# Kernel optimization log

Measured on AMD Instinct MI355X. Metric: run time of the kernel, lower is better.

The kernel has to match this reference:

```python
import jax, jax.numpy as jnp
import numpy as np

T, B, I, H = 2048, 32, 256, 256
KEEP = 0.75  # 1 - dropout_rate


def setup_inputs() -> dict:
    key = jax.random.key(0)
    ks = jax.random.split(key, 7)
    inp = jax.random.normal(ks[0], (T, B, I), dtype=jnp.float32)
    # variational dropout masks sampled once (Bernoulli(keep)), like the torch module
    zx = (jax.random.uniform(ks[1], (I,)) < KEEP).astype(jnp.float32)
    zh = (jax.random.uniform(ks[2], (H,)) < KEEP).astype(jnp.float32)
    # stacked gate weights in order [i, f, o, g]; scaled like nn.Linear default init
    s_w = 1.0 / np.sqrt(I)
    s_u = 1.0 / np.sqrt(H)
    W = jax.random.uniform(ks[3], (4 * H, I), minval=-s_w, maxval=s_w, dtype=jnp.float32)
    bW = jax.random.uniform(ks[4], (4 * H,), minval=-s_w, maxval=s_w, dtype=jnp.float32)
    U = jax.random.uniform(ks[5], (4 * H, H), minval=-s_u, maxval=s_u, dtype=jnp.float32)
    bU = jax.random.uniform(ks[6], (4 * H,), minval=-s_u, maxval=s_u, dtype=jnp.float32)
    return {"input": inp, "zx": zx, "zh": zh, "W": W, "bW": bW, "U": U, "bU": bU}


def reference(input, zx, zh, W, bW, U, bU):
    Bsz = input.shape[1]
    Hd = U.shape[1]

    def step(carry, x_t):
        h, c = carry
        x = x_t * zx          # [B, I] variational input dropout
        hm = h * zh           # [B, H] variational hidden dropout
        gates = x @ W.T + bW + hm @ U.T + bU   # [B, 4H]
        i, f, o, g = jnp.split(gates, 4, axis=-1)
        i = jax.nn.sigmoid(i)
        f = jax.nn.sigmoid(f)
        o = jax.nn.sigmoid(o)
        g = jnp.tanh(g)
        c_new = f * c + i * g
        h_new = o * jnp.tanh(c_new)
        return (h_new, c_new), h_new

    h0 = jnp.zeros((Bsz, Hd), dtype=input.dtype)
    c0 = jnp.zeros((Bsz, Hd), dtype=input.dtype)
    (h_t, c_t), hn = jax.lax.scan(step, (h0, c0), input)
    return hn, h_t, c_t
```

## Files before the change

kernel.cpp:

```cpp
#include <hip/hip_runtime.h>
#include <stdint.h>

typedef _Float16 half_t;
typedef _Float16 half2_t __attribute__((ext_vector_type(2)));
typedef _Float16 half8_t __attribute__((ext_vector_type(8)));
typedef float f32x4 __attribute__((ext_vector_type(4)));

#define TSEQ 2048
#define NB   32
#define HD   256
#define KC   224
#define KH   112
#define NQ   7
#define HN_ELEMS ((size_t)TSEQ*NB*HD)

static __device__ __forceinline__ int sdot4(uint32_t a, uint32_t b, int c) {
#if defined(__has_builtin)
#if __has_builtin(__builtin_amdgcn_sdot4)
  return __builtin_amdgcn_sdot4((int)a, (int)b, c, false);
#else
  int d;
  asm("v_dot4_i32_i8 %0, %1, %2, %3" : "=v"(d) : "v"(a), "v"(b), "v"(c));
  return d;
#endif
#else
  int d;
  asm("v_dot4_i32_i8 %0, %1, %2, %3" : "=v"(d) : "v"(a), "v"(b), "v"(c));
  return d;
#endif
}
static __device__ __forceinline__ float sigm_f(float x) {
  return __builtin_amdgcn_rcpf(1.0f + __expf(-x));
}
static __device__ __forceinline__ float tanh_f(float x) {
  return 2.0f * __builtin_amdgcn_rcpf(1.0f + __expf(-2.0f * x)) - 1.0f;
}
static __device__ __forceinline__ signed char q8(float v, float sc) {
  int q = (int)rintf(v * sc);
  q = q > 127 ? 127 : (q < -127 ? -127 : q);
  return (signed char)q;
}

__global__ void prep_kernel(const float* __restrict__ W, const float* __restrict__ U,
                            const float* __restrict__ bW, const float* __restrict__ bU,
                            const float* __restrict__ zx, const float* __restrict__ zh,
                            half_t* __restrict__ Wf16, signed char* __restrict__ Upk3b,
                            signed char* __restrict__ Ug4b, float* __restrict__ bias,
                            int* __restrict__ ipos,
                            half_t* __restrict__ hstate, float* __restrict__ cstate) {
  int tid = blockIdx.x * 256 + threadIdx.x;
  int n   = tid & 1023;
  int kcG = tid >> 10;

  int p = 0;
  for (int kk = 0; kk < kcG * 8; ++kk) p += (zh[kk] != 0.0f) ? 1 : 0;

  #pragma unroll
  for (int e = 0; e < 8; ++e) {
    int k = kcG * 8 + e;
    Wf16[(size_t)n * 256 + k] = (half_t)(W[n * 256 + k] * zx[k]);
    bool kept = (zh[k] != 0.0f);
    if (n == 0) ipos[k] = (kept && p < KC) ? p : -1;
    if (kept && p < KC) {
      float uv = U[n * 256 + k] * zh[k];
      signed char qv = q8(uv, 2032.0f);
      int kg = p / KH, pp = p % KH, q = pp >> 4, by = pp & 15;
      if (n < 768) {
        int c = n >> 8, j = n & 255;
        Upk3b[(((size_t)(c * 2 + kg) * NQ + q) * 256 + j) * 16 + by] = qv;
      } else {
        Ug4b[(((size_t)kg * NQ + q) * 256 + (n & 255)) * 16 + by] = qv;
      }
    }
    if (kept) ++p;
  }
  if (kcG == 0) bias[n] = bW[n] + bU[n];
  if (tid < NB * HD) { hstate[tid] = (half_t)0.0f; cstate[tid] = 0.0f; }
}

__global__ __launch_bounds__(256)
void gemm_kernel(const float* __restrict__ input, const half_t* __restrict__ Wf16,
                 const float* __restrict__ bias, half_t* __restrict__ gx, int row0) {
  const int tid  = threadIdx.x;
  const int lane = tid & 63;
  const int w    = tid >> 6;
  const int mr   = lane & 15;
  const int g    = lane >> 4;
  const int nb   = (blockIdx.x & 3) * 256;
  const int m0   = (blockIdx.x >> 2) * 64 + w * 16;

  f32x4 acc[16];
  #pragma unroll
  for (int nf = 0; nf < 16; ++nf) acc[nf] = (f32x4){0.f, 0.f, 0.f, 0.f};

  const float* arow = input + ((size_t)(row0 + m0 + mr)) * 256 + g * 8;
  #pragma unroll 1
  for (int kk = 0; kk < 8; ++kk) {
    float4 v0 = ((const float4*)(arow + kk * 32))[0];
    float4 v1 = ((const float4*)(arow + kk * 32))[1];
    half8_t a;
    a[0] = (half_t)v0.x; a[1] = (half_t)v0.y; a[2] = (half_t)v0.z; a[3] = (half_t)v0.w;
    a[4] = (half_t)v1.x; a[5] = (half_t)v1.y; a[6] = (half_t)v1.z; a[7] = (half_t)v1.w;
    const half_t* bbase = Wf16 + (size_t)(nb + mr) * 256 + kk * 32 + g * 8;
    #pragma unroll
    for (int nf = 0; nf < 16; ++nf) {
      uint4 bu = *(const uint4*)(bbase + (size_t)nf * 16 * 256);
      half8_t b = __builtin_bit_cast(half8_t, bu);
      acc[nf] = __builtin_amdgcn_mfma_f32_16x16x32_f16(a, b, acc[nf], 0, 0, 0);
    }
  }

  #pragma unroll
  for (int nf = 0; nf < 16; ++nf) {
    int n = nb + nf * 16 + mr;
    float bc = bias[n];
    #pragma unroll
    for (int i = 0; i < 4; ++i) {
      int r = m0 + g * 4 + i;
      gx[(size_t)r * 1024 + n] = (half_t)(acc[nf][i] + bc);
    }
  }
}

__global__ __launch_bounds__(512)
__attribute__((amdgpu_waves_per_eu(2, 2)))
void rec_kernel(const half_t* __restrict__ gx, const uint4* __restrict__ Upk3p,
                const uint4* __restrict__ Ug4p, const int* __restrict__ ipos,
                half_t* __restrict__ hstate, float* __restrict__ cstate,
                float* __restrict__ out, int tbase, int TB, int last,
                uint32_t rz) {
  __shared__ __align__(16) uint4 uglds[2 * NQ * 256];
  __shared__ __align__(16) uint4 hbv[2 * NQ];
  __shared__ __align__(16) int part[4 * 256];

  const int b   = blockIdx.x;
  const int tid = threadIdx.x;
  const int kg  = tid >> 8;
  const int j   = tid & 255;
  signed char* hbuf8 = (signed char*)hbv;

  #pragma unroll
  for (int i = 0; i < 7; ++i) uglds[i * 512 + tid] = Ug4p[i * 512 + tid];

  uint32_t upk0[4 * NQ], upk1[4 * NQ], upk2[4 * NQ];
  #pragma unroll
  for (int q = 0; q < NQ; ++q) {
    uint4 v = Upk3p[((size_t)(0 * 2 + kg) * NQ + q) * 256 + j];
    upk0[q * 4 + 0] = v.x ^ rz; upk0[q * 4 + 1] = v.y ^ rz;
    upk0[q * 4 + 2] = v.z ^ rz; upk0[q * 4 + 3] = v.w ^ rz;
  }
  #pragma unroll
  for (int q = 0; q < NQ; ++q) {
    uint4 v = Upk3p[((size_t)(1 * 2 + kg) * NQ + q) * 256 + j];
    upk1[q * 4 + 0] = v.x ^ rz; upk1[q * 4 + 1] = v.y ^ rz;
    upk1[q * 4 + 2] = v.z ^ rz; upk1[q * 4 + 3] = v.w ^ rz;
  }
  #pragma unroll
  for (int q = 0; q < NQ; ++q) {
    uint4 v = Upk3p[((size_t)(2 * 2 + kg) * NQ + q) * 256 + j];
    upk2[q * 4 + 0] = v.x ^ rz; upk2[q * 4 + 1] = v.y ^ rz;
    upk2[q * 4 + 2] = v.z ^ rz; upk2[q * 4 + 3] = v.w ^ rz;
  }

  if (tid < KC) hbuf8[tid] = 0;
  __syncthreads();

  const int ip = (kg == 0) ? ipos[j] : -1;

  float cc = 0.f, hprev = 0.f;
  half_t g0 = (half_t)0.f, g1 = g0, g2 = g0, g3 = g0;
  half_t n0 = g0, n1 = g0, n2 = g0, n3 = g0;
  const half_t* gpn = gx + (size_t)b * 1024 + j;
  float* outp = out + ((size_t)tbase * NB + b) * HD + j;
  if (kg == 0) {
    cc = cstate[b * HD + j];
    float h0 = (float)hstate[b * HD + j];
    hprev = h0;
    if (ip >= 0) hbuf8[ip] = (signed char)(int)rintf(h0 * 127.0f);
    g0 = gpn[0]; g1 = gpn[256]; g2 = gpn[512]; g3 = gpn[768];
  }
  gpn += (size_t)NB * 1024;
  __syncthreads();

  const float s = 0.0625f / 16129.0f;
  #pragma unroll 1
  for (int t = 0; t < TB; ++t) {
    if (kg == 0) {
      if (t > 0) { outp[-(int)(NB * HD)] = hprev; }
      if (t + 1 < TB) {
        n0 = gpn[0]; n1 = gpn[256]; n2 = gpn[512]; n3 = gpn[768];
      }
    }
    gpn += (size_t)NB * 1024;

    int a0 = 0, a1 = 0, a2 = 0, a3 = 0;
    const uint4* hp8 = hbv + kg * NQ;
    const uint4* ugp = uglds + (size_t)kg * NQ * 256 + j;
    #pragma unroll
    for (int q = 0; q < NQ; ++q) {
      uint4 hv = hp8[q];
      uint4 ug = ugp[q * 256];
      a0 = sdot4(upk0[q * 4 + 0], hv.x, a0);
      a0 = sdot4(upk0[q * 4 + 1], hv.y, a0);
      a0 = sdot4(upk0[q * 4 + 2], hv.z, a0);
      a0 = sdot4(upk0[q * 4 + 3], hv.w, a0);
      a1 = sdot4(upk1[q * 4 + 0], hv.x, a1);
      a1 = sdot4(upk1[q * 4 + 1], hv.y, a1);
      a1 = sdot4(upk1[q * 4 + 2], hv.z, a1);
      a1 = sdot4(upk1[q * 4 + 3], hv.w, a1);
      a2 = sdot4(upk2[q * 4 + 0], hv.x, a2);
      a2 = sdot4(upk2[q * 4 + 1], hv.y, a2);
      a2 = sdot4(upk2[q * 4 + 2], hv.z, a2);
      a2 = sdot4(upk2[q * 4 + 3], hv.w, a2);
      a3 = sdot4(ug.x, hv.x, a3);
      a3 = sdot4(ug.y, hv.y, a3);
      a3 = sdot4(ug.z, hv.z, a3);
      a3 = sdot4(ug.w, hv.w, a3);
    }
    if (kg) {
      part[0 * 256 + j] = a0;
      part[1 * 256 + j] = a1;
      part[2 * 256 + j] = a2;
      part[3 * 256 + j] = a3;
    }
    __syncthreads();
    if (kg == 0) {
      float f0 = (float)(a0 + part[0 * 256 + j]) * s + (float)g0;
      float f1 = (float)(a1 + part[1 * 256 + j]) * s + (float)g1;
      float f2 = (float)(a2 + part[2 * 256 + j]) * s + (float)g2;
      float f3 = (float)(a3 + part[3 * 256 + j]) * s + (float)g3;
      float gi = sigm_f(f0), gf = sigm_f(f1), go = sigm_f(f2), gg = tanh_f(f3);
      cc = gf * cc + gi * gg;
      float h = go * tanh_f(cc);
      hprev = h;
      if (ip >= 0) hbuf8[ip] = (signed char)(int)rintf(h * 127.0f);
      g0 = n0; g1 = n1; g2 = n2; g3 = n3;
    }
    outp += (size_t)NB * HD;
    __syncthreads();
  }
  if (kg == 0) {
    outp[-(int)(NB * HD)] = hprev;
    hstate[b * HD + j] = (half_t)hprev;
    cstate[b * HD + j] = cc;
    if (last) {
      out[HN_ELEMS + (size_t)b * HD + j] = hprev;
      out[HN_ELEMS + (size_t)NB * HD + (size_t)b * HD + j] = cc;
    }
  }
}

extern "C" void kernel_launch(void* const* d_in, const int* in_sizes, int n_in,
                              void* d_out, int out_size, void* d_ws, size_t ws_size,
                              hipStream_t stream) {
  const float* input = (const float*)d_in[0];
  const float* zx    = (const float*)d_in[1];
  const float* zh    = (const float*)d_in[2];
  const float* W     = (const float*)d_in[3];
  const float* bW    = (const float*)d_in[4];
  const float* U     = (const float*)d_in[5];
  const float* bU    = (const float*)d_in[6];
  float* out = (float*)d_out;

  char* ws = (char*)d_ws;
  signed char* Upk3b = (signed char*)(ws);
  signed char* Ug4b  = (signed char*)(ws + (192 << 10));
  half_t* Wf16   = (half_t*)(ws + (256 << 10));
  float*  bias   = (float*) (ws + (768 << 10));
  half_t* hstate = (half_t*)(ws + (772 << 10));
  float*  cstate = (float*) (ws + (788 << 10));
  int*    ipos   = (int*)   (ws + (820 << 10));
  half_t* gx     = (half_t*)(ws + (1 << 20));

  uint32_t rz = (uint32_t)(in_sizes[1] >> 9);

  int TB = TSEQ;
  while (TB > 32 && (size_t)(1u << 20) + (size_t)TB * NB * 1024 * 2 > ws_size) TB >>= 1;

  prep_kernel<<<128, 256, 0, stream>>>(W, U, bW, bU, zx, zh,
                                       Wf16, Upk3b, Ug4b,
                                       bias, ipos, hstate, cstate);

  int nch = TSEQ / TB;
  for (int c = 0; c < nch; ++c) {
    int tbase = c * TB;
    gemm_kernel<<<(TB * NB / 64) * 4, 256, 0, stream>>>(input, Wf16, bias, gx,
                                                        tbase * NB);
    rec_kernel<<<NB, 512, 0, stream>>>(gx, (const uint4*)Upk3b, (const uint4*)Ug4b,
                                       ipos, hstate, cstate, out,
                                       tbase, TB, (c == nch - 1) ? 1 : 0, rz);
  }
}
```

Before: 1.877 ms.

## Reduce K-split partials with cross-lane permlane swap and double-buffer hidden state

Remaps threads so the two K-halves of each hidden unit sit in the same wave (lanes 0-31 and 32-63). The partial dot products are then combined with v_permlane32_swap instead of going through a shared-memory partial buffer. The hidden-state LDS buffer is double-buffered by timestep parity, which removes one __syncthreads per step. Both halves now compute the gate nonlinearities redundantly, trading some extra ALU work for less LDS traffic and fewer barriers on the serial recurrence.

```diff
diff --git a/kernel.cpp b/kernel.cpp
--- a/kernel.cpp
+++ b/kernel.cpp
@@ -28,6 +28,13 @@
   asm("v_dot4_i32_i8 %0, %1, %2, %3" : "=v"(d) : "v"(a), "v"(b), "v"(c));
   return d;
 #endif
+}
+static __device__ __forceinline__ int halfsum(int a) {
+  int y;
+  asm("v_mov_b32 %1, %0\n\t"
+      "v_permlane32_swap_b32 %0, %1"
+      : "+v"(a), "=&v"(y));
+  return a + y;
 }
 static __device__ __forceinline__ float sigm_f(float x) {
   return __builtin_amdgcn_rcpf(1.0f + __expf(-x));
@@ -130,14 +137,13 @@
                 float* __restrict__ out, int tbase, int TB, int last,
                 uint32_t rz) {
   __shared__ __align__(16) uint4 uglds[2 * NQ * 256];
-  __shared__ __align__(16) uint4 hbv[2 * NQ];
-  __shared__ __align__(16) int part[4 * 256];
-
-  const int b   = blockIdx.x;
-  const int tid = threadIdx.x;
-  const int kg  = tid >> 8;
-  const int j   = tid & 255;
-  signed char* hbuf8 = (signed char*)hbv;
+  __shared__ __align__(16) uint4 hb[2][2 * NQ];
+
+  const int b    = blockIdx.x;
+  const int tid  = threadIdx.x;
+  const int lane = tid & 63;
+  const int kg   = lane >> 5;
+  const int j    = (tid >> 6) * 32 + (lane & 31);
 
   #pragma unroll
   for (int i = 0; i < 7; ++i) uglds[i * 512 + tid] = Ug4p[i * 512 + tid];
@@ -162,39 +168,34 @@
     upk2[q * 4 + 2] = v.z ^ rz; upk2[q * 4 + 3] = v.w ^ rz;
   }
 
-  if (tid < KC) hbuf8[tid] = 0;
+  if (tid < 2 * KC) ((signed char*)hb)[tid] = 0;
   __syncthreads();
 
-  const int ip = (kg == 0) ? ipos[j] : -1;
-
-  float cc = 0.f, hprev = 0.f;
-  half_t g0 = (half_t)0.f, g1 = g0, g2 = g0, g3 = g0;
-  half_t n0 = g0, n1 = g0, n2 = g0, n3 = g0;
+  const int ip = ipos[j];
+
+  float cc = cstate[b * HD + j];
+  float hprev = (float)hstate[b * HD + j];
+  if (kg == 0 && ip >= 0)
+    ((signed char*)hb[0])[ip] = (signed char)(int)rintf(hprev * 127.0f);
+
   const half_t* gpn = gx + (size_t)b * 1024 + j;
   float* outp = out + ((size_t)tbase * NB + b) * HD + j;
-  if (kg == 0) {
-    cc = cstate[b * HD + j];
-    float h0 = (float)hstate[b * HD + j];
-    hprev = h0;
-    if (ip >= 0) hbuf8[ip] = (signed char)(int)rintf(h0 * 127.0f);
-    g0 = gpn[0]; g1 = gpn[256]; g2 = gpn[512]; g3 = gpn[768];
-  }
+  half_t g0 = gpn[0], g1 = gpn[256], g2 = gpn[512], g3 = gpn[768];
+  half_t n0 = g0, n1 = g1, n2 = g2, n3 = g3;
   gpn += (size_t)NB * 1024;
   __syncthreads();
 
   const float s = 0.0625f / 16129.0f;
   #pragma unroll 1
   for (int t = 0; t < TB; ++t) {
-    if (kg == 0) {
-      if (t > 0) { outp[-(int)(NB * HD)] = hprev; }
-      if (t + 1 < TB) {
-        n0 = gpn[0]; n1 = gpn[256]; n2 = gpn[512]; n3 = gpn[768];
-      }
+    if (kg == 0 && t > 0) outp[-(int)(NB * HD)] = hprev;
+    if (t + 1 < TB) {
+      n0 = gpn[0]; n1 = gpn[256]; n2 = gpn[512]; n3 = gpn[768];
     }
     gpn += (size_t)NB * 1024;
 
     int a0 = 0, a1 = 0, a2 = 0, a3 = 0;
-    const uint4* hp8 = hbv + kg * NQ;
+    const uint4* hp8 = hb[t & 1] + kg * NQ;
     const uint4* ugp = uglds + (size_t)kg * NQ * 256 + j;
     #pragma unroll
     for (int q = 0; q < NQ; ++q) {
@@ -217,25 +218,20 @@
       a3 = sdot4(ug.z, hv.z, a3);
       a3 = sdot4(ug.w, hv.w, a3);
     }
-    if (kg) {
-      part[0 * 256 + j] = a0;
-      part[1 * 256 + j] = a1;
-      part[2 * 256 + j] = a2;
-      part[3 * 256 + j] = a3;
-    }
-    __syncthreads();
-    if (kg == 0) {
-      float f0 = (float)(a0 + part[0 * 256 + j]) * s + (float)g0;
-      float f1 = (float)(a1 + part[1 * 256 + j]) * s + (float)g1;
-      float f2 = (float)(a2 + part[2 * 256 + j]) * s + (float)g2;
-      float f3 = (float)(a3 + part[3 * 256 + j]) * s + (float)g3;
-      float gi = sigm_f(f0), gf = sigm_f(f1), go = sigm_f(f2), gg = tanh_f(f3);
-      cc = gf * cc + gi * gg;
-      float h = go * tanh_f(cc);
-      hprev = h;
-      if (ip >= 0) hbuf8[ip] = (signed char)(int)rintf(h * 127.0f);
-      g0 = n0; g1 = n1; g2 = n2; g3 = n3;
-    }
+    a0 = halfsum(a0); a1 = halfsum(a1);
+    a2 = halfsum(a2); a3 = halfsum(a3);
+
+    float f0 = (float)a0 * s + (float)g0;
+    float f1 = (float)a1 * s + (float)g1;
+    float f2 = (float)a2 * s + (float)g2;
+    float f3 = (float)a3 * s + (float)g3;
+    float gi = sigm_f(f0), gf = sigm_f(f1), go = sigm_f(f2), gg = tanh_f(f3);
+    cc = gf * cc + gi * gg;
+    float h = go * tanh_f(cc);
+    hprev = h;
+    if (kg == 0 && ip >= 0)
+      ((signed char*)hb[(t & 1) ^ 1])[ip] = (signed char)(int)rintf(h * 127.0f);
+    g0 = n0; g1 = n1; g2 = n2; g3 = n3;
     outp += (size_t)NB * HD;
     __syncthreads();
   }
```

After: 2.265 ms. 1.21x slower.

## Fuse input GEMM into recurrent kernel with flag-based producer-consumer overlap

Applied to the files above, without the earlier changes.

The separate input-projection GEMM launch and the recurrent launch are merged into one grid. The first 32 blocks run the recurrence and the rest compute gx tiles. Each GEMM block publishes completion through an atomic counter per two timesteps, and the recurrent blocks spin on these flags before reading gx. The aim is to hide the GEMM time behind the serial recurrence instead of running the two in sequence. In exchange it depends on the recurrent blocks being resident alongside the GEMM blocks, adds spin-wait overhead, and pads LDS to limit how many GEMM blocks can co-reside on a CU.

```diff
diff --git a/kernel.cpp b/kernel.cpp
--- a/kernel.cpp
+++ b/kernel.cpp
@@ -78,65 +78,77 @@
   if (tid < NB * HD) { hstate[tid] = (half_t)0.0f; cstate[tid] = 0.0f; }
 }
 
-__global__ __launch_bounds__(256)
-void gemm_kernel(const float* __restrict__ input, const half_t* __restrict__ Wf16,
-                 const float* __restrict__ bias, half_t* __restrict__ gx, int row0) {
-  const int tid  = threadIdx.x;
-  const int lane = tid & 63;
-  const int w    = tid >> 6;
-  const int mr   = lane & 15;
-  const int g    = lane >> 4;
-  const int nb   = (blockIdx.x & 3) * 256;
-  const int m0   = (blockIdx.x >> 2) * 64 + w * 16;
-
-  f32x4 acc[16];
-  #pragma unroll
-  for (int nf = 0; nf < 16; ++nf) acc[nf] = (f32x4){0.f, 0.f, 0.f, 0.f};
-
-  const float* arow = input + ((size_t)(row0 + m0 + mr)) * 256 + g * 8;
-  #pragma unroll 1
-  for (int kk = 0; kk < 8; ++kk) {
-    float4 v0 = ((const float4*)(arow + kk * 32))[0];
-    float4 v1 = ((const float4*)(arow + kk * 32))[1];
-    half8_t a;
-    a[0] = (half_t)v0.x; a[1] = (half_t)v0.y; a[2] = (half_t)v0.z; a[3] = (half_t)v0.w;
-    a[4] = (half_t)v1.x; a[5] = (half_t)v1.y; a[6] = (half_t)v1.z; a[7] = (half_t)v1.w;
-    const half_t* bbase = Wf16 + (size_t)(nb + mr) * 256 + kk * 32 + g * 8;
-    #pragma unroll
-    for (int nf = 0; nf < 16; ++nf) {
-      uint4 bu = *(const uint4*)(bbase + (size_t)nf * 16 * 256);
-      half8_t b = __builtin_bit_cast(half8_t, bu);
-      acc[nf] = __builtin_amdgcn_mfma_f32_16x16x32_f16(a, b, acc[nf], 0, 0, 0);
-    }
-  }
-
-  #pragma unroll
-  for (int nf = 0; nf < 16; ++nf) {
-    int n = nb + nf * 16 + mr;
-    float bc = bias[n];
-    #pragma unroll
-    for (int i = 0; i < 4; ++i) {
-      int r = m0 + g * 4 + i;
-      gx[(size_t)r * 1024 + n] = (half_t)(acc[nf][i] + bc);
-    }
-  }
+__global__ void zero_flags_kernel(int* __restrict__ flags) {
+  flags[blockIdx.x * 256 + threadIdx.x] = 0;
 }
 
 __global__ __launch_bounds__(512)
 __attribute__((amdgpu_waves_per_eu(2, 2)))
-void rec_kernel(const half_t* __restrict__ gx, const uint4* __restrict__ Upk3p,
-                const uint4* __restrict__ Ug4p, const int* __restrict__ ipos,
-                half_t* __restrict__ hstate, float* __restrict__ cstate,
-                float* __restrict__ out, int tbase, int TB, int last,
-                uint32_t rz) {
+void fused_kernel(const float* __restrict__ input, const half_t* __restrict__ Wf16,
+                  const float* __restrict__ bias, half_t* __restrict__ gx,
+                  const uint4* __restrict__ Upk3p, const uint4* __restrict__ Ug4p,
+                  const int* __restrict__ ipos,
+                  half_t* __restrict__ hstate, float* __restrict__ cstate,
+                  float* __restrict__ out, int* __restrict__ flags,
+                  int row0, int tbase, int TB, int last, uint32_t rz) {
   __shared__ __align__(16) uint4 uglds[2 * NQ * 256];
   __shared__ __align__(16) uint4 hbv[2 * NQ];
   __shared__ __align__(16) int part[4 * 256];
-
-  const int b   = blockIdx.x;
+  __shared__ __align__(16) uint4 pad1b[1600];
+
   const int tid = threadIdx.x;
-  const int kg  = tid >> 8;
-  const int j   = tid & 255;
+  if ((int)blockIdx.x < 0) pad1b[tid] = uglds[tid];
+
+  if (blockIdx.x >= NB) {
+    const int bid = blockIdx.x - NB;
+    if (tid < 256) {
+      const int lane = tid & 63;
+      const int w    = tid >> 6;
+      const int mr   = lane & 15;
+      const int g    = lane >> 4;
+      const int nb   = (bid & 3) * 256;
+      const int m0   = (bid >> 2) * 64 + w * 16;
+
+      f32x4 acc[16];
+      #pragma unroll
+      for (int nf = 0; nf < 16; ++nf) acc[nf] = (f32x4){0.f, 0.f, 0.f, 0.f};
+
+      const float* arow = input + ((size_t)(row0 + m0 + mr)) * 256 + g * 8;
+      #pragma unroll 1
+      for (int kk = 0; kk < 8; ++kk) {
+        float4 v0 = ((const float4*)(arow + kk * 32))[0];
+        float4 v1 = ((const float4*)(arow + kk * 32))[1];
+        half8_t a;
+        a[0] = (half_t)v0.x; a[1] = (half_t)v0.y; a[2] = (half_t)v0.z; a[3] = (half_t)v0.w;
+        a[4] = (half_t)v1.x; a[5] = (half_t)v1.y; a[6] = (half_t)v1.z; a[7] = (half_t)v1.w;
+        const half_t* bbase = Wf16 + (size_t)(nb + mr) * 256 + kk * 32 + g * 8;
+        #pragma unroll
+        for (int nf = 0; nf < 16; ++nf) {
+          uint4 bu = *(const uint4*)(bbase + (size_t)nf * 16 * 256);
+          half8_t b = __builtin_bit_cast(half8_t, bu);
+          acc[nf] = __builtin_amdgcn_mfma_f32_16x16x32_f16(a, b, acc[nf], 0, 0, 0);
+        }
+      }
+      #pragma unroll
+      for (int nf = 0; nf < 16; ++nf) {
+        int n = nb + nf * 16 + mr;
+        float bc = bias[n];
+        #pragma unroll
+        for (int i = 0; i < 4; ++i) {
+          int r = m0 + g * 4 + i;
+          gx[(size_t)r * 1024 + n] = (half_t)(acc[nf][i] + bc);
+        }
+      }
+    }
+    __threadfence();
+    __syncthreads();
+    if (tid == 0) atomicAdd(&flags[bid >> 2], 1);
+    return;
+  }
+
+  const int b  = blockIdx.x;
+  const int kg = tid >> 8;
+  const int j  = tid & 255;
   signed char* hbuf8 = (signed char*)hbv;
 
   #pragma unroll
@@ -177,18 +189,25 @@
     float h0 = (float)hstate[b * HD + j];
     hprev = h0;
     if (ip >= 0) hbuf8[ip] = (signed char)(int)rintf(h0 * 127.0f);
+    while (__hip_atomic_load(&flags[0], __ATOMIC_ACQUIRE, __HIP_MEMORY_SCOPE_AGENT) < 4)
+      __builtin_amdgcn_s_sleep(8);
+    __threadfence();
     g0 = gpn[0]; g1 = gpn[256]; g2 = gpn[512]; g3 = gpn[768];
   }
   gpn += (size_t)NB * 1024;
   __syncthreads();
 
   const float s = 0.0625f / 16129.0f;
+  int fvn = 4;
   #pragma unroll 1
   for (int t = 0; t < TB; ++t) {
+    const half_t* gcur = gpn;
     if (kg == 0) {
-      if (t > 0) { outp[-(int)(NB * HD)] = hprev; }
+      if (t > 0) outp[-(int)(NB * HD)] = hprev;
       if (t + 1 < TB) {
-        n0 = gpn[0]; n1 = gpn[256]; n2 = gpn[512]; n3 = gpn[768];
+        fvn = __hip_atomic_load(&flags[(t + 1) >> 1], __ATOMIC_RELAXED,
+                                __HIP_MEMORY_SCOPE_AGENT);
+        n0 = gcur[0]; n1 = gcur[256]; n2 = gcur[512]; n3 = gcur[768];
       }
     }
     gpn += (size_t)NB * 1024;
@@ -225,6 +244,13 @@
     }
     __syncthreads();
     if (kg == 0) {
+      if (t + 1 < TB && fvn < 4) {
+        while (__hip_atomic_load(&flags[(t + 1) >> 1], __ATOMIC_ACQUIRE,
+                                 __HIP_MEMORY_SCOPE_AGENT) < 4)
+          __builtin_amdgcn_s_sleep(8);
+        __threadfence();
+        n0 = gcur[0]; n1 = gcur[256]; n2 = gcur[512]; n3 = gcur[768];
+      }
       float f0 = (float)(a0 + part[0 * 256 + j]) * s + (float)g0;
       float f1 = (float)(a1 + part[1 * 256 + j]) * s + (float)g1;
       float f2 = (float)(a2 + part[2 * 256 + j]) * s + (float)g2;
@@ -270,6 +296,7 @@
   half_t* hstate = (half_t*)(ws + (772 << 10));
   float*  cstate = (float*) (ws + (788 << 10));
   int*    ipos   = (int*)   (ws + (820 << 10));
+  int*    flags  = (int*)   (ws + (824 << 10));
   half_t* gx     = (half_t*)(ws + (1 << 20));
 
   uint32_t rz = (uint32_t)(in_sizes[1] >> 9);
@@ -284,10 +311,12 @@
   int nch = TSEQ / TB;
   for (int c = 0; c < nch; ++c) {
     int tbase = c * TB;
-    gemm_kernel<<<(TB * NB / 64) * 4, 256, 0, stream>>>(input, Wf16, bias, gx,
-                                                        tbase * NB);
-    rec_kernel<<<NB, 512, 0, stream>>>(gx, (const uint4*)Upk3b, (const uint4*)Ug4b,
-                                       ipos, hstate, cstate, out,
-                                       tbase, TB, (c == nch - 1) ? 1 : 0, rz);
-  }
-}
+    int gemm_blocks = (TB * NB / 64) * 4;
+    zero_flags_kernel<<<4, 256, 0, stream>>>(flags);
+    fused_kernel<<<NB + gemm_blocks, 512, 0, stream>>>(
+        input, Wf16, bias, gx,
+        (const uint4*)Upk3b, (const uint4*)Ug4b, ipos,
+        hstate, cstate, out, flags,
+        tbase * NB, tbase, TB, (c == nch - 1) ? 1 : 0, rz);
+  }
+}
```

Measured after the change: 2.248 ms. 1.2x slower.
